# Optimization experiments

Measured on AMD Instinct MI355X. Metric: run time of the kernel, lower is better.

The kernel has to match this reference:

```python
import jax, jax.numpy as jnp
import numpy as np

DIM = 128
HEADS = 4
DIM_HEAD = 32
HIDDEN = HEADS * DIM_HEAD  # 128
EPS = 1e-5


def setup_inputs() -> dict:
    key = jax.random.key(0)
    ks = jax.random.split(key, 5)
    x = jax.random.normal(ks[0], (32, DIM, 64, 64), dtype=jnp.float32)
    # 1x1 convs are channel matmuls
    Wqkv = jax.random.normal(ks[1], (HIDDEN * 3, DIM), dtype=jnp.float32) * (1.0 / np.sqrt(DIM))
    Wout = jax.random.normal(ks[2], (DIM, HIDDEN), dtype=jnp.float32) * (1.0 / np.sqrt(HIDDEN))
    bout = jnp.zeros((DIM,), dtype=jnp.float32)
    ln_w = jnp.ones((DIM,), dtype=jnp.float32)
    ln_b = jnp.zeros((DIM,), dtype=jnp.float32)
    return {"x": x, "Wqkv": Wqkv, "Wout": Wout, "bout": bout, "ln_w": ln_w, "ln_b": ln_b}


def reference(x, Wqkv, Wout, bout, ln_w, ln_b):
    b, c, h, w = x.shape
    n = h * w
    xf = x.reshape(b, c, n)  # b c n
    qkv = jnp.einsum('oc,bcn->bon', Wqkv, xf)  # b (3*hidden) n
    q, k, v = jnp.split(qkv, 3, axis=1)
    # b (h d) n -> b h d n
    q = q.reshape(b, HEADS, DIM_HEAD, n)
    k = k.reshape(b, HEADS, DIM_HEAD, n)
    v = v.reshape(b, HEADS, DIM_HEAD, n)
    q = jax.nn.softmax(q, axis=-2)  # over feature dim d
    k = jax.nn.softmax(k, axis=-1)  # over spatial dim n
    context = jnp.einsum('bhdn,bhen->bhde', k, v)
    out = jnp.einsum('bhde,bhdn->bhen', context, q)  # b h e n
    out = out.reshape(b, HIDDEN, n)
    out = jnp.einsum('oc,bcn->bon', Wout, out) + bout[None, :, None]
    out = out.reshape(b, DIM, h, w)
    # LayerNorm2d over channel dim, biased variance
    mean = jnp.mean(out, axis=1, keepdims=True)
    var = jnp.var(out, axis=1, keepdims=True)
    out = (out - mean) / jnp.sqrt(var + EPS) * ln_w[None, :, None, None] + ln_b[None, :, None, None]
    return out
```

## Files before the change

kernel.cpp:

```cpp
#include <hip/hip_runtime.h>
#include <stdint.h>


constexpr int B_   = 32;
constexpr int C_   = 128;
constexpr int N_   = 4096;
constexpr int O3_  = 384;
constexpr int NSUB = 8;
constexpr int TPB_ = 8;

using short8  = __attribute__((ext_vector_type(8))) short;
using short4v = __attribute__((ext_vector_type(4))) short;
using float4v = __attribute__((ext_vector_type(4))) float;

__device__ __forceinline__ unsigned short bf16_rne(float f) {
    union { float f; uint32_t u; } v; v.f = f;
    uint32_t u = v.u;
    u += 0x7FFFu + ((u >> 16) & 1u);
    return (unsigned short)(u >> 16);
}
__device__ __forceinline__ float bf2f(unsigned short h) {
    union { uint32_t u; float f; } v; v.u = ((uint32_t)h) << 16; return v.f;
}

constexpr size_t OFF_WQ   = 0;
constexpr size_t OFF_WO   = 98304;
constexpr size_t OFF_SP   = 131072;
constexpr size_t OFF_CTXP = 262144;
constexpr size_t OFF_CTXN = 4456448;
constexpr size_t OFF_WBIG = 4718592;
constexpr size_t OFF_QSM  = 5767168;

__global__ __launch_bounds__(256) void k0_prep(const float* __restrict__ Wqkv,
                                               const float* __restrict__ Wout,
                                               unsigned short* __restrict__ wq,
                                               unsigned short* __restrict__ wo) {
    int t = blockIdx.x * 256 + threadIdx.x;
    if (t < O3_ * C_) wq[t] = bf16_rne(Wqkv[t]);
    if (t < C_ * C_)  wo[t] = bf16_rne(Wout[t]);
}

__global__ __launch_bounds__(1024) void k1_qkv(const float* __restrict__ x,
                                               const unsigned short* __restrict__ wq,
                                               unsigned short* __restrict__ qsm,
                                               float* __restrict__ ctx_part,
                                               float* __restrict__ S_part) {
    __shared__ __align__(16) unsigned short xs0[64 * 136];
    __shared__ __align__(16) unsigned short xs1[64 * 136];
    __shared__ __align__(16) unsigned short ek[128 * 72];
    __shared__ __align__(16) unsigned short vsh[128 * 72];

    const int b    = blockIdx.y;
    const int tblk = blockIdx.x;
    const int tid  = threadIdx.x;

    const int lane = tid & 63;
    const int wv   = tid >> 6;
    const int l15  = lane & 15;
    const int quad = lane >> 4;

    const float4v zero = {0.f, 0.f, 0.f, 0.f};

    short8 wfa[8];
    if (wv < 12) {
        const unsigned short* wqp = wq + (wv * 32 + l15) * C_ + quad * 8;
        #pragma unroll
        for (int kk = 0; kk < 4; kk++) {
            wfa[kk]     = *(const short8*)(wqp + kk * 32);
            wfa[4 + kk] = *(const short8*)(wqp + 16 * C_ + kk * 32);
        }
    }

    const int sid = tid & 255;
    const int snl = sid & 63;
    const int scg = sid >> 6;
    const float* xbase = x + ((size_t)b * C_ + (size_t)scg * 32) * N_ + snl;
    float xv[32];
    short8 c16[4];
    auto load_x = [&](int s) {
        const float* xp = xbase + (tblk * NSUB + s) * 64;
        #pragma unroll
        for (int i = 0; i < 32; i++) xv[i] = xp[(size_t)i * N_];
    };
    auto conv_x = [&]() {
        #pragma unroll
        for (int ii = 0; ii < 4; ii++) {
            short8 v8;
            #pragma unroll
            for (int j = 0; j < 8; j++) v8[j] = (short)bf16_rne(xv[ii * 8 + j]);
            c16[ii] = v8;
        }
    };
    auto store_c = [&](unsigned short* xs) {
        unsigned short* dst = &xs[snl * 136 + scg * 32];
        #pragma unroll
        for (int ii = 0; ii < 4; ii++) *(short8*)(dst + ii * 8) = c16[ii];
    };

    if (wv >= 12) {
        load_x(0); conv_x(); store_c(xs0);
        load_x(1);
    }
    unsigned short* xs_cur = xs0;
    unsigned short* xs_nxt = xs1;

    float4v cacc = zero;
    float s_acc  = 0.f;
    const int ch  = wv >> 2;
    const int cdt = (wv >> 1) & 1;
    const int cet = wv & 1;

    for (int s = 0; s < NSUB; s++) {
        const int ns = (tblk * NSUB + s) * 64;
        __syncthreads();

        if (wv < 12) {
            #pragma unroll
            for (int ct = 0; ct < 4; ct++) {
                short8 bfx[4];
                #pragma unroll
                for (int kk = 0; kk < 4; kk++)
                    bfx[kk] = *(const short8*)&xs_cur[(ct * 16 + l15) * 136 + kk * 32 + quad * 8];
                float4v acc0 = zero, acc1 = zero;
                #pragma unroll
                for (int kk = 0; kk < 4; kk++) {
                    acc0 = __builtin_amdgcn_mfma_f32_16x16x32_bf16(wfa[kk],     bfx[kk], acc0, 0, 0, 0);
                    acc1 = __builtin_amdgcn_mfma_f32_16x16x32_bf16(wfa[4 + kk], bfx[kk], acc1, 0, 0, 0);
                }
                const int ncol = ct * 16 + l15;
                if (wv < 4) {
                    float e0[4], e1[4], z = 0.f;
                    #pragma unroll
                    for (int r = 0; r < 4; r++) {
                        e0[r] = __expf(acc0[r]); e1[r] = __expf(acc1[r]);
                        z += e0[r] + e1[r];
                    }
                    z += __shfl_xor(z, 16, 64);
                    z += __shfl_xor(z, 32, 64);
                    const float iz = 1.0f / z;
                    unsigned short* qp = qsm + ((size_t)b * N_ + ns + ncol) * C_ + wv * 32 + quad * 4;
                    short4v s0, s1;
                    #pragma unroll
                    for (int r = 0; r < 4; r++) {
                        s0[r] = (short)bf16_rne(e0[r] * iz);
                        s1[r] = (short)bf16_rne(e1[r] * iz);
                    }
                    *(short4v*)qp = s0;
                    *(short4v*)(qp + 16) = s1;
                } else if (wv < 8) {
                    const int row0 = (wv - 4) * 32 + quad * 4;
                    #pragma unroll
                    for (int r = 0; r < 4; r++) {
                        ek[(row0 + r) * 72 + ncol]      = bf16_rne(__expf(acc0[r]));
                        ek[(row0 + 16 + r) * 72 + ncol] = bf16_rne(__expf(acc1[r]));
                    }
                } else {
                    const int row0 = (wv - 8) * 32 + quad * 4;
                    #pragma unroll
                    for (int r = 0; r < 4; r++) {
                        vsh[(row0 + r) * 72 + ncol]      = bf16_rne(acc0[r]);
                        vsh[(row0 + 16 + r) * 72 + ncol] = bf16_rne(acc1[r]);
                    }
                }
            }
        } else {
            if (s + 1 < NSUB) { conv_x(); store_c(xs_nxt); }
            if (s + 2 < NSUB) load_x(s + 2);
        }
        __syncthreads();

        {
            const unsigned short* ap = &ek[(ch * 32 + cdt * 16 + l15) * 72 + quad * 8];
            const unsigned short* bp = &vsh[(ch * 32 + cet * 16 + l15) * 72 + quad * 8];
            #pragma unroll
            for (int kk = 0; kk < 2; kk++) {
                short8 a  = *(const short8*)(ap + kk * 32);
                short8 bb = *(const short8*)(bp + kk * 32);
                cacc = __builtin_amdgcn_mfma_f32_16x16x32_bf16(a, bb, cacc, 0, 0, 0);
            }
        }
        {
            const unsigned short* ep = &ek[(tid >> 3) * 72 + (tid & 7) * 8];
            short8 e0 = *(const short8*)ep;
            float ss = 0.f;
            #pragma unroll
            for (int j = 0; j < 8; j++) ss += bf2f((unsigned short)e0[j]);
            s_acc += ss;
        }
        { unsigned short* t = xs_cur; xs_cur = xs_nxt; xs_nxt = t; }
    }

    {
        float* cp = ctx_part + ((size_t)(b * TPB_ + tblk) << 12)
                  + ((ch * 32 + cdt * 16 + quad * 4) * 32 + cet * 16 + l15);
        #pragma unroll
        for (int r = 0; r < 4; r++) cp[r * 32] = cacc[r];
    }
    {
        float ss = s_acc;
        ss += __shfl_xor(ss, 1, 64);
        ss += __shfl_xor(ss, 2, 64);
        ss += __shfl_xor(ss, 4, 64);
        if ((tid & 7) == 0)
            S_part[(size_t)(b * TPB_ + tblk) * 128 + (tid >> 3)] = ss;
    }
}

__global__ __launch_bounds__(256) void k2a_reduce(const float* __restrict__ ctx_part,
                                                  const float* __restrict__ S_part,
                                                  unsigned short* __restrict__ ctxn) {
    __shared__ float Sinv[16];
    const int b     = blockIdx.x >> 3;
    const int chunk = blockIdx.x & 7;
    const int tid   = threadIdx.x;
    if (tid < 16) {
        const int hd = chunk * 16 + tid;
        float s = 0.f;
        #pragma unroll
        for (int t = 0; t < TPB_; t++)
            s += S_part[(size_t)(b * TPB_ + t) * 128 + hd];
        Sinv[tid] = 1.0f / s;
    }
    __syncthreads();
    #pragma unroll
    for (int j = 0; j < 2; j++) {
        const int ei = chunk * 512 + j * 256 + tid;
        float v = 0.f;
        #pragma unroll
        for (int t = 0; t < TPB_; t++)
            v += ctx_part[((size_t)(b * TPB_ + t) << 12) + ei];
        ctxn[(size_t)b * 4096 + ei] = bf16_rne(v * Sinv[(ei >> 5) - chunk * 16]);
    }
}

__global__ __launch_bounds__(512) void k2b_fold(const unsigned short* __restrict__ ctxn,
                                                const unsigned short* __restrict__ wo,
                                                unsigned short* __restrict__ wbig) {
    const int b   = blockIdx.x;
    const int tid = threadIdx.x;
    const int lane = tid & 63, wv = tid >> 6, l15 = lane & 15, quad = lane >> 4;
    const float4v zero = {0.f, 0.f, 0.f, 0.f};

    short8 a4[4], b8[8];
    #pragma unroll
    for (int h = 0; h < 4; h++)
        a4[h] = *(const short8*)(wo + (wv * 16 + l15) * C_ + h * 32 + quad * 8);
    #pragma unroll
    for (int ht = 0; ht < 8; ht++)
        b8[ht] = *(const short8*)(ctxn + (size_t)b * 4096
                                  + ((ht >> 1) * 32 + (ht & 1) * 16 + l15) * 32 + quad * 8);

    unsigned short* wb = wbig + (size_t)b * (C_ * C_);
    #pragma unroll
    for (int ht = 0; ht < 8; ht++) {
        float4v c4 = __builtin_amdgcn_mfma_f32_16x16x32_bf16(a4[ht >> 1], b8[ht], zero, 0, 0, 0);
        const int c     = wv * 4 + (ht >> 1);
        const int quadp = (ht & 1) * 2 + (l15 >> 3);
        #pragma unroll
        for (int r = 0; r < 4; r++)
            wb[((c * 64 + quadp * 16 + quad * 4 + r) << 3) + (l15 & 7)] = bf16_rne(c4[r]);
    }
}

__global__ __launch_bounds__(512) void k3_out(const unsigned short* __restrict__ qsm,
                                              const unsigned short* __restrict__ wbig,
                                              const float* __restrict__ bout,
                                              const float* __restrict__ lnw,
                                              const float* __restrict__ lnb,
                                              float* __restrict__ out) {
    __shared__ __align__(16) unsigned short wls[16384];
    __shared__ float lnp[384];

    const int b    = blockIdx.y;
    const int tseg = blockIdx.x;
    const int tid  = threadIdx.x;

    const int lane = tid & 63, wv = tid >> 6, l15 = lane & 15, quad = lane >> 4;
    const int nl = wv * 16 + l15;

    const float4v zero = {0.f, 0.f, 0.f, 0.f};
    const size_t n0base = (size_t)tseg * 256;

    short8 st[4];
    {
        const short8* src = (const short8*)(wbig + (size_t)b * (C_ * C_));
        #pragma unroll
        for (int i = 0; i < 4; i++) st[i] = src[i * 512 + tid];
    }
    if (tid < 128) {
        lnp[tid]       = bout[tid];
        lnp[128 + tid] = lnw[tid];
        lnp[256 + tid] = lnb[tid];
    }
    short8 bq[4], bqn[4];
    {
        const unsigned short* qp = qsm + ((size_t)b * N_ + n0base + nl) * C_ + quad * 8;
        #pragma unroll
        for (int kk = 0; kk < 4; kk++) bq[kk] = *(const short8*)(qp + kk * 32);
    }
    #pragma unroll
    for (int i = 0; i < 4; i++)
        *(short8*)&wls[(i * 512 + tid) * 8] = st[i];
    __syncthreads();

    #pragma unroll
    for (int t = 0; t < 2; t++) {
        const size_t n = n0base + t * 128 + nl;
        if (t == 0) {
            const unsigned short* qp = qsm + ((size_t)b * N_ + n0base + 128 + nl) * C_ + quad * 8;
            #pragma unroll
            for (int kk = 0; kk < 4; kk++) bqn[kk] = *(const short8*)(qp + kk * 32);
        }

        float4v acc[8];
        #pragma unroll
        for (int ot = 0; ot < 8; ot++) {
            float4v a = zero;
            #pragma unroll
            for (int kk = 0; kk < 4; kk++) {
                short8 w = *(const short8*)&wls[((ot * 4 + kk) * 64 + lane) * 8];
                a = __builtin_amdgcn_mfma_f32_16x16x32_bf16(w, bq[kk], a, 0, 0, 0);
            }
            acc[ot] = a;
        }

        float sum = 0.f, sq = 0.f;
        #pragma unroll
        for (int ot = 0; ot < 8; ot++) {
            #pragma unroll
            for (int r = 0; r < 4; r++) {
                const int o = ot * 16 + quad * 4 + r;
                const float y = acc[ot][r] + lnp[o];
                acc[ot][r] = y;
                sum += y; sq += y * y;
            }
        }
        sum += __shfl_xor(sum, 16, 64);
        sum += __shfl_xor(sum, 32, 64);
        sq  += __shfl_xor(sq, 16, 64);
        sq  += __shfl_xor(sq, 32, 64);
        const float mean = sum * (1.0f / 128.0f);
        const float var  = sq * (1.0f / 128.0f) - mean * mean;
        const float rstd = rsqrtf(var + 1e-5f);

        #pragma unroll
        for (int ot = 0; ot < 8; ot++) {
            #pragma unroll
            for (int r = 0; r < 4; r++) {
                const int o = ot * 16 + quad * 4 + r;
                out[((size_t)b * C_ + o) * N_ + n] = (acc[ot][r] - mean) * rstd * lnp[128 + o] + lnp[256 + o];
            }
        }

        #pragma unroll
        for (int kk = 0; kk < 4; kk++) bq[kk] = bqn[kk];
    }
}

extern "C" void kernel_launch(void* const* d_in, const int* in_sizes, int n_in,
                              void* d_out, int out_size, void* d_ws, size_t ws_size,
                              hipStream_t stream) {
    const float* x    = (const float*)d_in[0];
    const float* Wqkv = (const float*)d_in[1];
    const float* Wout = (const float*)d_in[2];
    const float* bout = (const float*)d_in[3];
    const float* lnw  = (const float*)d_in[4];
    const float* lnb  = (const float*)d_in[5];
    float* out = (float*)d_out;

    char* ws = (char*)d_ws;
    unsigned short* wq   = (unsigned short*)(ws + OFF_WQ);
    unsigned short* wo   = (unsigned short*)(ws + OFF_WO);
    float* S_part        = (float*)(ws + OFF_SP);
    float* ctx_part      = (float*)(ws + OFF_CTXP);
    unsigned short* ctxn = (unsigned short*)(ws + OFF_CTXN);
    unsigned short* wbig = (unsigned short*)(ws + OFF_WBIG);
    unsigned short* qsm  = (unsigned short*)(ws + OFF_QSM);

    k0_prep<<<192, 256, 0, stream>>>(Wqkv, Wout, wq, wo);
    k1_qkv<<<dim3(TPB_, B_), 1024, 0, stream>>>(x, wq, qsm, ctx_part, S_part);
    k2a_reduce<<<B_ * 8, 256, 0, stream>>>(ctx_part, S_part, ctxn);
    k2b_fold<<<B_, 512, 0, stream>>>(ctxn, wo, wbig);
    k3_out<<<dim3(16, B_), 512, 0, stream>>>(qsm, wbig, bout, lnw, lnb, out);
}
```

Before: 158.4 us.

## Double-buffer ek/vsh to pipeline context MFMA with next QKV step

Double-buffers the exp(k) and v shared tiles and software-pipelines the sub-tile loop. The context accumulation for step s-1 now runs in the same phase as the QKV projection for step s, so there is one barrier per iteration instead of two. This uses more LDS (about 36KB extra), which could reduce occupancy for a 1024-thread block, and it adds one extra loop iteration to drain the pipeline.

```diff
diff --git a/kernel.cpp b/kernel.cpp
--- a/kernel.cpp
+++ b/kernel.cpp
@@ -45,10 +45,9 @@
                                                unsigned short* __restrict__ qsm,
                                                float* __restrict__ ctx_part,
                                                float* __restrict__ S_part) {
-    __shared__ __align__(16) unsigned short xs0[64 * 136];
-    __shared__ __align__(16) unsigned short xs1[64 * 136];
-    __shared__ __align__(16) unsigned short ek[128 * 72];
-    __shared__ __align__(16) unsigned short vsh[128 * 72];
+    __shared__ __align__(16) unsigned short xs[2][64 * 136];
+    __shared__ __align__(16) unsigned short ek[2][128 * 72];
+    __shared__ __align__(16) unsigned short vsh[2][128 * 72];
 
     const int b    = blockIdx.y;
     const int tblk = blockIdx.x;
@@ -91,18 +90,16 @@
             c16[ii] = v8;
         }
     };
-    auto store_c = [&](unsigned short* xs) {
-        unsigned short* dst = &xs[snl * 136 + scg * 32];
+    auto store_c = [&](unsigned short* xsb) {
+        unsigned short* dst = &xsb[snl * 136 + scg * 32];
         #pragma unroll
         for (int ii = 0; ii < 4; ii++) *(short8*)(dst + ii * 8) = c16[ii];
     };
 
     if (wv >= 12) {
-        load_x(0); conv_x(); store_c(xs0);
+        load_x(0); conv_x(); store_c(xs[0]);
         load_x(1);
     }
-    unsigned short* xs_cur = xs0;
-    unsigned short* xs_nxt = xs1;
 
     float4v cacc = zero;
     float s_acc  = 0.f;
@@ -110,84 +107,84 @@
     const int cdt = (wv >> 1) & 1;
     const int cet = wv & 1;
 
-    for (int s = 0; s < NSUB; s++) {
-        const int ns = (tblk * NSUB + s) * 64;
+    for (int s = 0; s <= NSUB; s++) {
         __syncthreads();
-
-        if (wv < 12) {
-            #pragma unroll
-            for (int ct = 0; ct < 4; ct++) {
-                short8 bfx[4];
-                #pragma unroll
-                for (int kk = 0; kk < 4; kk++)
-                    bfx[kk] = *(const short8*)&xs_cur[(ct * 16 + l15) * 136 + kk * 32 + quad * 8];
-                float4v acc0 = zero, acc1 = zero;
-                #pragma unroll
-                for (int kk = 0; kk < 4; kk++) {
-                    acc0 = __builtin_amdgcn_mfma_f32_16x16x32_bf16(wfa[kk],     bfx[kk], acc0, 0, 0, 0);
-                    acc1 = __builtin_amdgcn_mfma_f32_16x16x32_bf16(wfa[4 + kk], bfx[kk], acc1, 0, 0, 0);
-                }
-                const int ncol = ct * 16 + l15;
-                if (wv < 4) {
-                    float e0[4], e1[4], z = 0.f;
-                    #pragma unroll
-                    for (int r = 0; r < 4; r++) {
-                        e0[r] = __expf(acc0[r]); e1[r] = __expf(acc1[r]);
-                        z += e0[r] + e1[r];
-                    }
-                    z += __shfl_xor(z, 16, 64);
-                    z += __shfl_xor(z, 32, 64);
-                    const float iz = 1.0f / z;
-                    unsigned short* qp = qsm + ((size_t)b * N_ + ns + ncol) * C_ + wv * 32 + quad * 4;
-                    short4v s0, s1;
-                    #pragma unroll
-                    for (int r = 0; r < 4; r++) {
-                        s0[r] = (short)bf16_rne(e0[r] * iz);
-                        s1[r] = (short)bf16_rne(e1[r] * iz);
-                    }
-                    *(short4v*)qp = s0;
-                    *(short4v*)(qp + 16) = s1;
-                } else if (wv < 8) {
-                    const int row0 = (wv - 4) * 32 + quad * 4;
-                    #pragma unroll
-                    for (int r = 0; r < 4; r++) {
-                        ek[(row0 + r) * 72 + ncol]      = bf16_rne(__expf(acc0[r]));
-                        ek[(row0 + 16 + r) * 72 + ncol] = bf16_rne(__expf(acc1[r]));
-                    }
-                } else {
-                    const int row0 = (wv - 8) * 32 + quad * 4;
-                    #pragma unroll
-                    for (int r = 0; r < 4; r++) {
-                        vsh[(row0 + r) * 72 + ncol]      = bf16_rne(acc0[r]);
-                        vsh[(row0 + 16 + r) * 72 + ncol] = bf16_rne(acc1[r]);
-                    }
-                }
-            }
-        } else {
-            if (s + 1 < NSUB) { conv_x(); store_c(xs_nxt); }
-            if (s + 2 < NSUB) load_x(s + 2);
-        }
-        __syncthreads();
-
-        {
-            const unsigned short* ap = &ek[(ch * 32 + cdt * 16 + l15) * 72 + quad * 8];
-            const unsigned short* bp = &vsh[(ch * 32 + cet * 16 + l15) * 72 + quad * 8];
+        const int cur = s & 1;
+        const int prv = cur ^ 1;
+
+        if (s > 0) {
+            const unsigned short* ap = &ek[prv][(ch * 32 + cdt * 16 + l15) * 72 + quad * 8];
+            const unsigned short* bp = &vsh[prv][(ch * 32 + cet * 16 + l15) * 72 + quad * 8];
             #pragma unroll
             for (int kk = 0; kk < 2; kk++) {
                 short8 a  = *(const short8*)(ap + kk * 32);
                 short8 bb = *(const short8*)(bp + kk * 32);
                 cacc = __builtin_amdgcn_mfma_f32_16x16x32_bf16(a, bb, cacc, 0, 0, 0);
             }
-        }
-        {
-            const unsigned short* ep = &ek[(tid >> 3) * 72 + (tid & 7) * 8];
+            const unsigned short* ep = &ek[prv][(tid >> 3) * 72 + (tid & 7) * 8];
             short8 e0 = *(const short8*)ep;
             float ss = 0.f;
             #pragma unroll
             for (int j = 0; j < 8; j++) ss += bf2f((unsigned short)e0[j]);
             s_acc += ss;
         }
-        { unsigned short* t = xs_cur; xs_cur = xs_nxt; xs_nxt = t; }
+
+        if (s < NSUB) {
+            const int ns = (tblk * NSUB + s) * 64;
+            if (wv < 12) {
+                #pragma unroll
+                for (int ct = 0; ct < 4; ct++) {
+                    short8 bfx[4];
+                    #pragma unroll
+                    for (int kk = 0; kk < 4; kk++)
+                        bfx[kk] = *(const short8*)&xs[cur][(ct * 16 + l15) * 136 + kk * 32 + quad * 8];
+                    float4v acc0 = zero, acc1 = zero;
+                    #pragma unroll
+                    for (int kk = 0; kk < 4; kk++) {
+                        acc0 = __builtin_amdgcn_mfma_f32_16x16x32_bf16(wfa[kk],     bfx[kk], acc0, 0, 0, 0);
+                        acc1 = __builtin_amdgcn_mfma_f32_16x16x32_bf16(wfa[4 + kk], bfx[kk], acc1, 0, 0, 0);
+                    }
+                    const int ncol = ct * 16 + l15;
+                    if (wv < 4) {
+                        float e0[4], e1[4], z = 0.f;
+                        #pragma unroll
+                        for (int r = 0; r < 4; r++) {
+                            e0[r] = __expf(acc0[r]); e1[r] = __expf(acc1[r]);
+                            z += e0[r] + e1[r];
+                        }
+                        z += __shfl_xor(z, 16, 64);
+                        z += __shfl_xor(z, 32, 64);
+                        const float iz = 1.0f / z;
+                        unsigned short* qp = qsm + ((size_t)b * N_ + ns + ncol) * C_ + wv * 32 + quad * 4;
+                        short4v s0, s1;
+                        #pragma unroll
+                        for (int r = 0; r < 4; r++) {
+                            s0[r] = (short)bf16_rne(e0[r] * iz);
+                            s1[r] = (short)bf16_rne(e1[r] * iz);
+                        }
+                        *(short4v*)qp = s0;
+                        *(short4v*)(qp + 16) = s1;
+                    } else if (wv < 8) {
+                        const int row0 = (wv - 4) * 32 + quad * 4;
+                        #pragma unroll
+                        for (int r = 0; r < 4; r++) {
+                            ek[cur][(row0 + r) * 72 + ncol]      = bf16_rne(__expf(acc0[r]));
+                            ek[cur][(row0 + 16 + r) * 72 + ncol] = bf16_rne(__expf(acc1[r]));
+                        }
+                    } else {
+                        const int row0 = (wv - 8) * 32 + quad * 4;
+                        #pragma unroll
+                        for (int r = 0; r < 4; r++) {
+                            vsh[cur][(row0 + r) * 72 + ncol]      = bf16_rne(acc0[r]);
+                            vsh[cur][(row0 + 16 + r) * 72 + ncol] = bf16_rne(acc1[r]);
+                        }
+                    }
+                }
+            } else {
+                if (s + 1 < NSUB) { conv_x(); store_c(xs[cur ^ 1]); }
+                if (s + 2 < NSUB) load_x(s + 2);
+            }
+        }
     }
 
     {
```

Result: no change. 161.4 us (+1.9%).
